# Kernel optimization log

Measured on AMD Instinct MI355X. Metric: run time of the kernel, lower is better.

The kernel has to match this reference:

```python
import jax, jax.numpy as jnp
import numpy as np
import math

D_MODEL = 1024
D_HIDDEN = 64


def setup_inputs() -> dict:
    key = jax.random.key(0)
    ks = jax.random.split(key, 9)
    s_in = 1.0 / math.sqrt(D_MODEL)
    s_h = 1.0 / math.sqrt(D_HIDDEN)
    return {
        "x": jax.random.normal(ks[0], (4, 4096, D_MODEL), dtype=jnp.float32),
        "Wq": jax.random.normal(ks[1], (D_HIDDEN, D_MODEL), dtype=jnp.float32) * s_in,
        "bq": jnp.zeros((D_HIDDEN,), dtype=jnp.float32),
        "Wk": jax.random.normal(ks[2], (D_HIDDEN, D_MODEL), dtype=jnp.float32) * s_in,
        "bk": jnp.zeros((D_HIDDEN,), dtype=jnp.float32),
        "Wov": jax.random.normal(ks[3], (D_HIDDEN, D_MODEL), dtype=jnp.float32) * s_in,
        "bov": jnp.zeros((D_HIDDEN,), dtype=jnp.float32),
        "Wo": jax.random.normal(ks[4], (D_MODEL, D_HIDDEN), dtype=jnp.float32) * s_h,
        "bo": jnp.zeros((D_MODEL,), dtype=jnp.float32),
    }


def reference(x, Wq, bq, Wk, bk, Wov, bov, Wo, bo):
    # x: [B, n_ctx, d_model]
    Q = x @ Wq.T + bq          # [B, n, d_hidden]
    K = x @ Wk.T + bk
    V = x @ Wov.T + bov
    n_ctx = x.shape[-2]
    # causal mask: -inf strictly above the diagonal (matches torch.triu diag=1)
    mask = jnp.triu(jnp.full((n_ctx, n_ctx), -jnp.inf, dtype=x.dtype), k=1)
    # NOTE: source divides by sqrt(d_model), not sqrt(d_hidden)
    scores = jnp.einsum("bqd,bkd->bqk", Q, K) / math.sqrt(D_MODEL)
    attn = jax.nn.softmax(scores + mask, axis=-1)  # [B, n, n]
    out = jnp.einsum("bqk,bkd->bqd", attn, V)      # [B, n, d_hidden]
    return out @ Wo.T + bo                          # [B, n, d_model]
```

## Files before the change

kernel.cpp:

```cpp
#include <hip/hip_runtime.h>

#define DM 1024
#define DH 64
#define NBATCH 4
#define NCTX 4096
#define MTOT (NBATCH*NCTX)

typedef __bf16 bf16x8 __attribute__((ext_vector_type(8)));
typedef float f32x4 __attribute__((ext_vector_type(4)));

#define MFMA16(a,b,c) __builtin_amdgcn_mfma_f32_16x16x32_bf16(a,b,c,0,0,0)

__device__ inline ushort f2bf(float f) {
  unsigned u = __builtin_bit_cast(unsigned, f);
  u += 0x7fffu + ((u >> 16) & 1u);
  return (ushort)(u >> 16);
}

__global__ __launch_bounds__(256) void wconv_kernel(
    const float* __restrict__ Wq, const float* __restrict__ Wk,
    const float* __restrict__ Wov, const float* __restrict__ Wo,
    ushort* __restrict__ wqkv, ushort* __restrict__ wo)
{
  int idx = (blockIdx.x * 256 + threadIdx.x) * 4;
  if (idx < 196608) {
    const float* src = (idx < 65536) ? (Wq + idx)
                     : (idx < 131072 ? (Wk + (idx - 65536)) : (Wov + (idx - 131072)));
    float4 v = *(const float4*)src;
    ushort4 o = { f2bf(v.x), f2bf(v.y), f2bf(v.z), f2bf(v.w) };
    *(ushort4*)(wqkv + idx) = o;
  } else {
    int j = idx - 196608;
    float4 v = *(const float4*)(Wo + j);
    ushort4 o = { f2bf(v.x), f2bf(v.y), f2bf(v.z), f2bf(v.w) };
    *(ushort4*)(wo + j) = o;
  }
}

__global__ __launch_bounds__(256) void qkv_kernel(
    const float* __restrict__ x, const ushort* __restrict__ wqkv,
    const float* __restrict__ bq, const float* __restrict__ bk,
    const float* __restrict__ bov,
    ushort* __restrict__ Qo, ushort* __restrict__ Ko, ushort* __restrict__ Vt)
{
  __shared__ __attribute__((aligned(16))) ushort xs[32 * 1024];
  const int tid  = threadIdx.x;
  const int lane = tid & 63;
  const int wave = tid >> 6;
  const int mt   = wave & 1;
  const int nh   = wave >> 1;
  const int l15  = lane & 15;
  const int l4   = lane >> 4;
  const int row0 = blockIdx.x * 32;

  #pragma unroll 8
  for (int i = 0; i < 32; ++i) {
    int f4  = tid + i * 256;
    int row = f4 >> 8;
    int c4  = f4 & 255;
    float4 v = *(const float4*)(x + (size_t)(row0 + row) * DM + c4 * 4);
    ushort4 o = { f2bf(v.x), f2bf(v.y), f2bf(v.z), f2bf(v.w) };
    int byteoff = row * 2048 + ((c4 * 8) ^ ((row & 7) << 4));
    *(ushort4*)((char*)xs + byteoff) = o;
  }
  __syncthreads();

  f32x4 acc[6] = {};
  const int arow = mt * 16 + l15;
  const int aswz = (arow & 7) << 4;
  #pragma unroll 4
  for (int cc = 0; cc < 32; ++cc) {
    bf16x8 a = *(const bf16x8*)((const char*)xs + arow * 2048 + ((cc * 64 + l4 * 16) ^ aswz));
    #pragma unroll
    for (int i = 0; i < 6; ++i) {
      int brow = (nh * 6 + i) * 16 + l15;
      bf16x8 b = *(const bf16x8*)(wqkv + (size_t)brow * DM + cc * 32 + l4 * 8);
      acc[i] = MFMA16(a, b, acc[i]);
    }
  }

  const float qscale = 1.4426950408889634f / 32.0f;
  #pragma unroll
  for (int i = 0; i < 6; ++i) {
    int nt = nh * 6 + i;
    int n  = nt * 16 + l15;
    #pragma unroll
    for (int r = 0; r < 4; ++r) {
      int grow = row0 + mt * 16 + l4 * 4 + r;
      float v = acc[i][r];
      if (n < 64) {
        Qo[(size_t)grow * 64 + n] = f2bf((v + bq[n]) * qscale);
      } else if (n < 128) {
        int nn = n - 64;
        Ko[(size_t)grow * 64 + nn] = f2bf(v + bk[nn]);
      } else {
        int nn = n - 128;
        int b = grow >> 12, pos = grow & 4095;
        Vt[((size_t)b * 64 + nn) * NCTX + pos] = f2bf(v + bov[nn]);
      }
    }
  }
}

__global__ __launch_bounds__(256) void attn_kernel(
    const ushort* __restrict__ Q, const ushort* __restrict__ K,
    const ushort* __restrict__ Vt, const ushort* __restrict__ wo,
    const float* __restrict__ bo, float* __restrict__ out)
{
  __shared__ __attribute__((aligned(16))) ushort Ps[4][16 * 64];
  __shared__ __attribute__((aligned(16))) float cO[3][16][64];
  __shared__ float cM[3][16], cL[3][16];
  __shared__ __attribute__((aligned(16))) ushort O_lds[16 * 64];

  const int tid  = threadIdx.x;
  const int lane = tid & 63;
  const int wave = tid >> 6;
  const int l15  = lane & 15;
  const int l4   = lane >> 4;

  const int bb    = blockIdx.x & 3;
  const int strip = 255 - (blockIdx.x >> 2);
  const int qs0   = strip * 16;

  const ushort* Qb  = Q  + (size_t)bb * NCTX * 64;
  const ushort* Kb  = K  + (size_t)bb * NCTX * 64;
  const ushort* Vtb = Vt + (size_t)bb * 64 * NCTX;

  bf16x8 qf[2];
  #pragma unroll
  for (int c = 0; c < 2; ++c)
    qf[c] = *(const bf16x8*)(Qb + (size_t)(qs0 + l15) * 64 + c * 32 + l4 * 8);

  const int ntot = (qs0 + 79) >> 6;
  const int cpw  = (ntot + 3) >> 2;
  const int t0 = wave * cpw;
  const int t1 = min(ntot, t0 + cpw);

  float m_run = -1e30f, l_run = 0.f;
  f32x4 accO[4] = {};
  ushort* Pw = (ushort*)Ps[wave];
  const int swz = (l15 & 7) << 4;

  for (int it = t0; it < t1; ++it) {
    const int kv0 = it * 64;
    f32x4 s4[4] = {};
    __builtin_amdgcn_s_setprio(1);
    #pragma unroll
    for (int c = 0; c < 2; ++c) {
      #pragma unroll
      for (int nt = 0; nt < 4; ++nt) {
        bf16x8 kf = *(const bf16x8*)(Kb + (size_t)(kv0 + nt * 16 + l15) * 64 + c * 32 + l4 * 8);
        s4[nt] = MFMA16(kf, qf[c], s4[nt]);
      }
    }
    __builtin_amdgcn_s_setprio(0);
    if (kv0 + 63 > qs0) {
      #pragma unroll
      for (int nt = 0; nt < 4; ++nt) {
        #pragma unroll
        for (int r = 0; r < 4; ++r) {
          int kvg = kv0 + nt * 16 + l4 * 4 + r;
          if (kvg > qs0 + l15) s4[nt][r] = -1e30f;
        }
      }
    }
    float mx = -1e30f;
    #pragma unroll
    for (int nt = 0; nt < 4; ++nt)
      #pragma unroll
      for (int r = 0; r < 4; ++r) mx = fmaxf(mx, s4[nt][r]);
    mx = fmaxf(mx, __shfl_xor(mx, 16));
    mx = fmaxf(mx, __shfl_xor(mx, 32));
    float mn = fmaxf(m_run, mx);
    float alpha = exp2f(m_run - mn);
    m_run = mn;
    float sm = 0.f;
    #pragma unroll
    for (int nt = 0; nt < 4; ++nt)
      #pragma unroll
      for (int r = 0; r < 4; ++r) {
        float p = exp2f(s4[nt][r] - mn);
        s4[nt][r] = p; sm += p;
      }
    sm += __shfl_xor(sm, 16);
    sm += __shfl_xor(sm, 32);
    l_run = l_run * alpha + sm;
    #pragma unroll
    for (int r = 0; r < 4; ++r) {
      float ar = __shfl(alpha, (lane & 48) | (l4 * 4 + r));
      #pragma unroll
      for (int dt = 0; dt < 4; ++dt) accO[dt][r] *= ar;
    }
    #pragma unroll
    for (int nt = 0; nt < 4; ++nt) {
      ushort4 pw = { f2bf(s4[nt][0]), f2bf(s4[nt][1]), f2bf(s4[nt][2]), f2bf(s4[nt][3]) };
      int byteoff = l15 * 128 + (((nt * 32 + l4 * 8)) ^ swz);
      *(ushort4*)((char*)Pw + byteoff) = pw;
    }
    #pragma unroll
    for (int c = 0; c < 2; ++c) {
      bf16x8 pa = *(const bf16x8*)((const char*)Pw + l15 * 128 + ((c * 64 + l4 * 16) ^ swz));
      __builtin_amdgcn_s_setprio(1);
      #pragma unroll
      for (int dt = 0; dt < 4; ++dt) {
        bf16x8 vb = *(const bf16x8*)(Vtb + (size_t)(dt * 16 + l15) * NCTX + kv0 + c * 32 + l4 * 8);
        accO[dt] = MFMA16(pa, vb, accO[dt]);
      }
      __builtin_amdgcn_s_setprio(0);
    }
  }

  if (wave != 0) {
    #pragma unroll
    for (int dt = 0; dt < 4; ++dt)
      #pragma unroll
      for (int r = 0; r < 4; ++r)
        cO[wave - 1][l4 * 4 + r][dt * 16 + l15] = accO[dt][r];
    if (l4 == 0) { cM[wave - 1][l15] = m_run; cL[wave - 1][l15] = l_run; }
  }
  __syncthreads();
  if (wave == 0) {
    float Ms = m_run;
    #pragma unroll
    for (int w = 0; w < 3; ++w) Ms = fmaxf(Ms, cM[w][l15]);
    float f0 = exp2f(m_run - Ms);
    float fw[3];
    float L = l_run * f0;
    #pragma unroll
    for (int w = 0; w < 3; ++w) { fw[w] = exp2f(cM[w][l15] - Ms); L += cL[w][l15] * fw[w]; }
    float invL = 1.0f / L;
    #pragma unroll
    for (int r = 0; r < 4; ++r) {
      int q = l4 * 4 + r;
      int src = (lane & 48) | q;
      float f0r = __shfl(f0, src);
      float iLr = __shfl(invL, src);
      float fwr[3];
      #pragma unroll
      for (int w = 0; w < 3; ++w) fwr[w] = __shfl(fw[w], src);
      int qswz = (q & 7) << 4;
      #pragma unroll
      for (int dt = 0; dt < 4; ++dt) {
        float o = accO[dt][r] * f0r;
        #pragma unroll
        for (int w = 0; w < 3; ++w) o += fwr[w] * cO[w][q][dt * 16 + l15];
        int byteoff = q * 128 + ((dt * 32 + l15 * 2) ^ qswz);
        *(ushort*)((char*)O_lds + byteoff) = f2bf(o * iLr);
      }
    }
  }
  __syncthreads();

  bf16x8 oa[2];
  const int oswz = (l15 & 7) << 4;
  #pragma unroll
  for (int c = 0; c < 2; ++c)
    oa[c] = *(const bf16x8*)((const char*)O_lds + l15 * 128 + ((c * 64 + l4 * 16) ^ oswz));

  f32x4 pacc[16] = {};
  #pragma unroll
  for (int nt = 0; nt < 16; ++nt) {
    int n = wave * 256 + nt * 16 + l15;
    #pragma unroll
    for (int c = 0; c < 2; ++c) {
      bf16x8 b = *(const bf16x8*)(wo + (size_t)n * 64 + c * 32 + l4 * 8);
      pacc[nt] = MFMA16(oa[c], b, pacc[nt]);
    }
  }
  const size_t orow0 = (size_t)bb * NCTX + qs0;
  #pragma unroll
  for (int nt = 0; nt < 16; ++nt) {
    int n = wave * 256 + nt * 16 + l15;
    float bv = bo[n];
    #pragma unroll
    for (int r = 0; r < 4; ++r) {
      out[(orow0 + l4 * 4 + r) * 1024 + n] = pacc[nt][r] + bv;
    }
  }
}

extern "C" void kernel_launch(void* const* d_in, const int* in_sizes, int n_in,
                              void* d_out, int out_size, void* d_ws, size_t ws_size,
                              hipStream_t stream) {
  const float* x   = (const float*)d_in[0];
  const float* Wq  = (const float*)d_in[1];
  const float* bq  = (const float*)d_in[2];
  const float* Wk  = (const float*)d_in[3];
  const float* bk  = (const float*)d_in[4];
  const float* Wov = (const float*)d_in[5];
  const float* bov = (const float*)d_in[6];
  const float* Wo  = (const float*)d_in[7];
  const float* bo  = (const float*)d_in[8];
  float* out = (float*)d_out;

  char* ws = (char*)d_ws;
  ushort* wqkv = (ushort*)(ws);
  ushort* wo   = (ushort*)(ws + 393216);
  ushort* Qw   = (ushort*)(ws + 524288);
  ushort* Kw   = (ushort*)(ws + 524288 + 2097152);
  ushort* Vtw  = (ushort*)(ws + 524288 + 2 * 2097152);

  wconv_kernel<<<256, 256, 0, stream>>>(Wq, Wk, Wov, Wo, wqkv, wo);
  qkv_kernel<<<512, 256, 0, stream>>>(x, wqkv, bq, bk, bov, Qw, Kw, Vtw);
  attn_kernel<<<1024, 256, 0, stream>>>(Qw, Kw, Vtw, wo, bo, out);
}
```

Baseline: 249.1 us.

## Pre-pack Q/K/V and weights into MFMA fragment order; process two KV tiles per iteration

Weights, Q, K and V are now written in a packed layout matching the MFMA operand fragment order, so each lane loads one contiguous 16-byte chunk and a wave reads a contiguous 1 KB block. This targets uncoalesced, strided global loads in the QKV GEMM, the attention inner loop and the output projection. The attention loop also processes two 64-wide KV tiles per iteration with a doubled P staging buffer, which halves the softmax rescale overhead and gives more independent loads per iteration. The cost is more register pressure and scattered scalar stores in the QKV epilogue.

```diff
diff --git a/kernel.cpp b/kernel.cpp
--- a/kernel.cpp
+++ b/kernel.cpp
@@ -17,10 +17,11 @@
   return (ushort)(u >> 16);
 }
 
+
 __global__ __launch_bounds__(256) void wconv_kernel(
     const float* __restrict__ Wq, const float* __restrict__ Wk,
     const float* __restrict__ Wov, const float* __restrict__ Wo,
-    ushort* __restrict__ wqkv, ushort* __restrict__ wo)
+    ushort* __restrict__ wqkvp, ushort* __restrict__ wop)
 {
   int idx = (blockIdx.x * 256 + threadIdx.x) * 4;
   if (idx < 196608) {
@@ -28,20 +29,24 @@
                      : (idx < 131072 ? (Wk + (idx - 65536)) : (Wov + (idx - 131072)));
     float4 v = *(const float4*)src;
     ushort4 o = { f2bf(v.x), f2bf(v.y), f2bf(v.z), f2bf(v.w) };
-    *(ushort4*)(wqkv + idx) = o;
+    int row = idx >> 10, col = idx & 1023;
+    int T = row >> 4, l15 = row & 15, C = col >> 5, l4 = (col >> 3) & 3, j = col & 7;
+    *(ushort4*)(wqkvp + (((T * 32 + C) * 64 + l4 * 16 + l15) * 8 + j)) = o;
   } else {
-    int j = idx - 196608;
-    float4 v = *(const float4*)(Wo + j);
+    int k = idx - 196608;
+    float4 v = *(const float4*)(Wo + k);
     ushort4 o = { f2bf(v.x), f2bf(v.y), f2bf(v.z), f2bf(v.w) };
-    *(ushort4*)(wo + j) = o;
+    int row = k >> 6, col = k & 63;
+    int T = row >> 4, l15 = row & 15, C = col >> 5, l4 = (col >> 3) & 3, j = col & 7;
+    *(ushort4*)(wop + (((T * 2 + C) * 64 + l4 * 16 + l15) * 8 + j)) = o;
   }
 }
 
 __global__ __launch_bounds__(256) void qkv_kernel(
-    const float* __restrict__ x, const ushort* __restrict__ wqkv,
+    const float* __restrict__ x, const ushort* __restrict__ wqkvp,
     const float* __restrict__ bq, const float* __restrict__ bk,
     const float* __restrict__ bov,
-    ushort* __restrict__ Qo, ushort* __restrict__ Ko, ushort* __restrict__ Vt)
+    ushort* __restrict__ Qp, ushort* __restrict__ Kp, ushort* __restrict__ Vp)
 {
   __shared__ __attribute__((aligned(16))) ushort xs[32 * 1024];
   const int tid  = threadIdx.x;
@@ -73,8 +78,7 @@
     bf16x8 a = *(const bf16x8*)((const char*)xs + arow * 2048 + ((cc * 64 + l4 * 16) ^ aswz));
     #pragma unroll
     for (int i = 0; i < 6; ++i) {
-      int brow = (nh * 6 + i) * 16 + l15;
-      bf16x8 b = *(const bf16x8*)(wqkv + (size_t)brow * DM + cc * 32 + l4 * 8);
+      bf16x8 b = *(const bf16x8*)(wqkvp + (((size_t)(nh * 6 + i) * 32 + cc) * 64 + lane) * 8);
       acc[i] = MFMA16(a, b, acc[i]);
     }
   }
@@ -82,32 +86,35 @@
   const float qscale = 1.4426950408889634f / 32.0f;
   #pragma unroll
   for (int i = 0; i < 6; ++i) {
-    int nt = nh * 6 + i;
-    int n  = nt * 16 + l15;
+    int n = (nh * 6 + i) * 16 + l15;
     #pragma unroll
     for (int r = 0; r < 4; ++r) {
       int grow = row0 + mt * 16 + l4 * 4 + r;
       float v = acc[i][r];
       if (n < 64) {
-        Qo[(size_t)grow * 64 + n] = f2bf((v + bq[n]) * qscale);
+        size_t a = (((size_t)(grow >> 4) * 2 + (n >> 5)) * 64 + ((n >> 3) & 3) * 16 + (grow & 15)) * 8 + (n & 7);
+        Qp[a] = f2bf((v + bq[n]) * qscale);
       } else if (n < 128) {
         int nn = n - 64;
-        Ko[(size_t)grow * 64 + nn] = f2bf(v + bk[nn]);
+        size_t a = (((size_t)(grow >> 4) * 2 + (nn >> 5)) * 64 + ((nn >> 3) & 3) * 16 + (grow & 15)) * 8 + (nn & 7);
+        Kp[a] = f2bf(v + bk[nn]);
       } else {
-        int nn = n - 128;
+        int d = n - 128;
         int b = grow >> 12, pos = grow & 4095;
-        Vt[((size_t)b * 64 + nn) * NCTX + pos] = f2bf(v + bov[nn]);
+        size_t a = (size_t)b * 262144 +
+                   (((size_t)(d >> 4) * 128 + (pos >> 5)) * 64 + ((pos >> 3) & 3) * 16 + (d & 15)) * 8 + (pos & 7);
+        Vp[a] = f2bf(v + bov[d]);
       }
     }
   }
 }
 
 __global__ __launch_bounds__(256) void attn_kernel(
-    const ushort* __restrict__ Q, const ushort* __restrict__ K,
-    const ushort* __restrict__ Vt, const ushort* __restrict__ wo,
+    const ushort* __restrict__ Qp, const ushort* __restrict__ Kp,
+    const ushort* __restrict__ Vp, const ushort* __restrict__ wop,
     const float* __restrict__ bo, float* __restrict__ out)
 {
-  __shared__ __attribute__((aligned(16))) ushort Ps[4][16 * 64];
+  __shared__ __attribute__((aligned(16))) ushort Ps[4][16 * 128];
   __shared__ __attribute__((aligned(16))) float cO[3][16][64];
   __shared__ float cM[3][16], cL[3][16];
   __shared__ __attribute__((aligned(16))) ushort O_lds[16 * 64];
@@ -122,14 +129,13 @@
   const int strip = 255 - (blockIdx.x >> 2);
   const int qs0   = strip * 16;
 
-  const ushort* Qb  = Q  + (size_t)bb * NCTX * 64;
-  const ushort* Kb  = K  + (size_t)bb * NCTX * 64;
-  const ushort* Vtb = Vt + (size_t)bb * 64 * NCTX;
+  const size_t vbase = (size_t)bb * 262144;
+  const int Tq = bb * 256 + strip;
 
   bf16x8 qf[2];
   #pragma unroll
   for (int c = 0; c < 2; ++c)
-    qf[c] = *(const bf16x8*)(Qb + (size_t)(qs0 + l15) * 64 + c * 32 + l4 * 8);
+    qf[c] = *(const bf16x8*)(Qp + (((size_t)Tq * 2 + c) * 64 + lane) * 8);
 
   const int ntot = (qs0 + 79) >> 6;
   const int cpw  = (ntot + 3) >> 2;
@@ -141,32 +147,34 @@
   ushort* Pw = (ushort*)Ps[wave];
   const int swz = (l15 & 7) << 4;
 
-  for (int it = t0; it < t1; ++it) {
-    const int kv0 = it * 64;
-    f32x4 s4[4] = {};
+  int it = t0;
+  for (; it + 1 < t1; it += 2) {
+    const int kv0 = it * 64, kv1 = kv0 + 64;
+    const int Tk0 = bb * 256 + (kv0 >> 4);
+    f32x4 s4[8] = {};
     __builtin_amdgcn_s_setprio(1);
     #pragma unroll
     for (int c = 0; c < 2; ++c) {
       #pragma unroll
-      for (int nt = 0; nt < 4; ++nt) {
-        bf16x8 kf = *(const bf16x8*)(Kb + (size_t)(kv0 + nt * 16 + l15) * 64 + c * 32 + l4 * 8);
+      for (int nt = 0; nt < 8; ++nt) {
+        bf16x8 kf = *(const bf16x8*)(Kp + (((size_t)(Tk0 + nt) * 2 + c) * 64 + lane) * 8);
         s4[nt] = MFMA16(kf, qf[c], s4[nt]);
       }
     }
     __builtin_amdgcn_s_setprio(0);
-    if (kv0 + 63 > qs0) {
+    if (kv1 + 63 > qs0) {
       #pragma unroll
       for (int nt = 0; nt < 4; ++nt) {
         #pragma unroll
         for (int r = 0; r < 4; ++r) {
-          int kvg = kv0 + nt * 16 + l4 * 4 + r;
-          if (kvg > qs0 + l15) s4[nt][r] = -1e30f;
+          int kvg = kv1 + nt * 16 + l4 * 4 + r;
+          if (kvg > qs0 + l15) s4[4 + nt][r] = -1e30f;
         }
       }
     }
     float mx = -1e30f;
     #pragma unroll
-    for (int nt = 0; nt < 4; ++nt)
+    for (int nt = 0; nt < 8; ++nt)
       #pragma unroll
       for (int r = 0; r < 4; ++r) mx = fmaxf(mx, s4[nt][r]);
     mx = fmaxf(mx, __shfl_xor(mx, 16));
@@ -176,7 +184,7 @@
     m_run = mn;
     float sm = 0.f;
     #pragma unroll
-    for (int nt = 0; nt < 4; ++nt)
+    for (int nt = 0; nt < 8; ++nt)
       #pragma unroll
       for (int r = 0; r < 4; ++r) {
         float p = exp2f(s4[nt][r] - mn);
@@ -193,17 +201,86 @@
     }
     #pragma unroll
     for (int nt = 0; nt < 4; ++nt) {
+      ushort4 pwA = { f2bf(s4[nt][0]), f2bf(s4[nt][1]), f2bf(s4[nt][2]), f2bf(s4[nt][3]) };
+      ushort4 pwB = { f2bf(s4[4+nt][0]), f2bf(s4[4+nt][1]), f2bf(s4[4+nt][2]), f2bf(s4[4+nt][3]) };
+      *(ushort4*)((char*)Pw + l15 * 256 + ((nt * 32 + l4 * 8) ^ swz)) = pwA;
+      *(ushort4*)((char*)Pw + l15 * 256 + ((128 + nt * 32 + l4 * 8) ^ swz)) = pwB;
+    }
+    #pragma unroll
+    for (int c = 0; c < 4; ++c) {
+      bf16x8 pa = *(const bf16x8*)((const char*)Pw + l15 * 256 + ((c * 64 + l4 * 16) ^ swz));
+      __builtin_amdgcn_s_setprio(1);
+      #pragma unroll
+      for (int dt = 0; dt < 4; ++dt) {
+        bf16x8 vb = *(const bf16x8*)(Vp + vbase + (((size_t)dt * 128 + (kv0 >> 5) + c) * 64 + lane) * 8);
+        accO[dt] = MFMA16(pa, vb, accO[dt]);
+      }
+      __builtin_amdgcn_s_setprio(0);
+    }
+  }
+  if (it < t1) {
+    const int kv0 = it * 64;
+    const int Tk0 = bb * 256 + (kv0 >> 4);
+    f32x4 s4[4] = {};
+    __builtin_amdgcn_s_setprio(1);
+    #pragma unroll
+    for (int c = 0; c < 2; ++c) {
+      #pragma unroll
+      for (int nt = 0; nt < 4; ++nt) {
+        bf16x8 kf = *(const bf16x8*)(Kp + (((size_t)(Tk0 + nt) * 2 + c) * 64 + lane) * 8);
+        s4[nt] = MFMA16(kf, qf[c], s4[nt]);
+      }
+    }
+    __builtin_amdgcn_s_setprio(0);
+    if (kv0 + 63 > qs0) {
+      #pragma unroll
+      for (int nt = 0; nt < 4; ++nt) {
+        #pragma unroll
+        for (int r = 0; r < 4; ++r) {
+          int kvg = kv0 + nt * 16 + l4 * 4 + r;
+          if (kvg > qs0 + l15) s4[nt][r] = -1e30f;
+        }
+      }
+    }
+    float mx = -1e30f;
+    #pragma unroll
+    for (int nt = 0; nt < 4; ++nt)
+      #pragma unroll
+      for (int r = 0; r < 4; ++r) mx = fmaxf(mx, s4[nt][r]);
+    mx = fmaxf(mx, __shfl_xor(mx, 16));
+    mx = fmaxf(mx, __shfl_xor(mx, 32));
+    float mn = fmaxf(m_run, mx);
+    float alpha = exp2f(m_run - mn);
+    m_run = mn;
+    float sm = 0.f;
+    #pragma unroll
+    for (int nt = 0; nt < 4; ++nt)
+      #pragma unroll
+      for (int r = 0; r < 4; ++r) {
+        float p = exp2f(s4[nt][r] - mn);
+        s4[nt][r] = p; sm += p;
+      }
+    sm += __shfl_xor(sm, 16);
+    sm += __shfl_xor(sm, 32);
+    l_run = l_run * alpha + sm;
+    #pragma unroll
+    for (int r = 0; r < 4; ++r) {
+      float ar = __shfl(alpha, (lane & 48) | (l4 * 4 + r));
+      #pragma unroll
+      for (int dt = 0; dt < 4; ++dt) accO[dt][r] *= ar;
+    }
+    #pragma unroll
+    for (int nt = 0; nt < 4; ++nt) {
       ushort4 pw = { f2bf(s4[nt][0]), f2bf(s4[nt][1]), f2bf(s4[nt][2]), f2bf(s4[nt][3]) };
-      int byteoff = l15 * 128 + (((nt * 32 + l4 * 8)) ^ swz);
-      *(ushort4*)((char*)Pw + byteoff) = pw;
+      *(ushort4*)((char*)Pw + l15 * 256 + ((nt * 32 + l4 * 8) ^ swz)) = pw;
     }
     #pragma unroll
     for (int c = 0; c < 2; ++c) {
-      bf16x8 pa = *(const bf16x8*)((const char*)Pw + l15 * 128 + ((c * 64 + l4 * 16) ^ swz));
+      bf16x8 pa = *(const bf16x8*)((const char*)Pw + l15 * 256 + ((c * 64 + l4 * 16) ^ swz));
       __builtin_amdgcn_s_setprio(1);
       #pragma unroll
       for (int dt = 0; dt < 4; ++dt) {
-        bf16x8 vb = *(const bf16x8*)(Vtb + (size_t)(dt * 16 + l15) * NCTX + kv0 + c * 32 + l4 * 8);
+        bf16x8 vb = *(const bf16x8*)(Vp + vbase + (((size_t)dt * 128 + (kv0 >> 5) + c) * 64 + lane) * 8);
         accO[dt] = MFMA16(pa, vb, accO[dt]);
       }
       __builtin_amdgcn_s_setprio(0);
@@ -260,10 +337,9 @@
   f32x4 pacc[16] = {};
   #pragma unroll
   for (int nt = 0; nt < 16; ++nt) {
-    int n = wave * 256 + nt * 16 + l15;
     #pragma unroll
     for (int c = 0; c < 2; ++c) {
-      bf16x8 b = *(const bf16x8*)(wo + (size_t)n * 64 + c * 32 + l4 * 8);
+      bf16x8 b = *(const bf16x8*)(wop + (((size_t)(wave * 16 + nt) * 2 + c) * 64 + lane) * 8);
       pacc[nt] = MFMA16(oa[c], b, pacc[nt]);
     }
   }
@@ -294,13 +370,13 @@
   float* out = (float*)d_out;
 
   char* ws = (char*)d_ws;
-  ushort* wqkv = (ushort*)(ws);
-  ushort* wo   = (ushort*)(ws + 393216);
-  ushort* Qw   = (ushort*)(ws + 524288);
-  ushort* Kw   = (ushort*)(ws + 524288 + 2097152);
-  ushort* Vtw  = (ushort*)(ws + 524288 + 2 * 2097152);
-
-  wconv_kernel<<<256, 256, 0, stream>>>(Wq, Wk, Wov, Wo, wqkv, wo);
-  qkv_kernel<<<512, 256, 0, stream>>>(x, wqkv, bq, bk, bov, Qw, Kw, Vtw);
-  attn_kernel<<<1024, 256, 0, stream>>>(Qw, Kw, Vtw, wo, bo, out);
-}
+  ushort* wqkvp = (ushort*)(ws);
+  ushort* wop   = (ushort*)(ws + 393216);
+  ushort* Qpw   = (ushort*)(ws + 524288);
+  ushort* Kpw   = (ushort*)(ws + 524288 + 2097152);
+  ushort* Vpw   = (ushort*)(ws + 524288 + 2 * 2097152);
+
+  wconv_kernel<<<256, 256, 0, stream>>>(Wq, Wk, Wov, Wo, wqkvp, wop);
+  qkv_kernel<<<512, 256, 0, stream>>>(x, wqkvp, bq, bk, bov, Qpw, Kpw, Vpw);
+  attn_kernel<<<1024, 256, 0, stream>>>(Qpw, Kpw, Vpw, wop, bo, out);
+}
```

Result: faster. 200.4 us (-19.6%).
